# Kernel tuning notes

Measured on AMD Instinct MI355X. Metric: run time of the kernel, lower is better.

Reference implementation:

```python
import jax, jax.numpy as jnp
import numpy as np


def setup_inputs() -> dict:
    key = jax.random.key(0)
    B, S, H, D = 4, 2048, 16, 64
    kq, kk, kv, kl = jax.random.split(key, 4)
    q = jax.random.normal(kq, (B, S, H, D), dtype=jnp.float32)
    k = jax.random.normal(kk, (B, S, H, D), dtype=jnp.float32)
    v = jax.random.normal(kv, (B, S, H, D), dtype=jnp.float32)
    # varlen: each sequence has a valid prefix length in [S//2, S]
    lengths = jax.random.randint(kl, (B,), S // 2, S + 1)
    key_padding_mask = jnp.arange(S)[None, :] < lengths[:, None]  # [B, S] bool
    return {"q": q, "k": k, "v": v, "key_padding_mask": key_padding_mask}


def reference(q, k, v, key_padding_mask):
    # q,k,v: [B, S, H, D]; key_padding_mask: [B, S] (True = valid key/value token).
    # Equivalent math of ring varlen flash attention: every query attends to all
    # valid (unpadded) key positions of its sequence; padded keys are excluded.
    D = q.shape[-1]
    scale = 1.0 / np.sqrt(D).astype(np.float32)
    scores = jnp.einsum('bshd,bthd->bhst', q, k) * scale  # [B, H, S, S]
    neg = jnp.finfo(scores.dtype).min
    scores = jnp.where(key_padding_mask[:, None, None, :], scores, neg)
    probs = jax.nn.softmax(scores, axis=-1)
    context = jnp.einsum('bhst,bthd->bshd', probs, v)  # [B, S, H, D]
    return context
```

## Files before the change

kernel.cpp:

```cpp
#include <hip/hip_runtime.h>

#define BB 4
#define SS 2048
#define HH 16
#define DD 64

#define NQW 8
#define QW  32
#define QB  (NQW*QW)
#define KVB 32

#define KRS 144
#define VRS 80

typedef short bf16x8 __attribute__((ext_vector_type(8)));
typedef float f32x16 __attribute__((ext_vector_type(16)));

__device__ __forceinline__ unsigned cvtpk(float lo, float hi){
    unsigned r;
    asm("v_cvt_pk_bf16_f32 %0, %1, %2" : "=v"(r) : "v"(lo), "v"(hi));
    return r;
}

#if __has_builtin(__builtin_amdgcn_exp2f)
#define EXP2F(x) __builtin_amdgcn_exp2f(x)
#else
__device__ __forceinline__ float exp2_asm(float x){
    float r; asm("v_exp_f32 %0, %1\n\ts_nop 0" : "=v"(r) : "v"(x)); return r;
}
#define EXP2F(x) exp2_asm(x)
#endif

union FragU { unsigned u[4]; bf16x8 v; };

__global__ __launch_bounds__(512)
void attn_mfma(const float* __restrict__ qg, const float* __restrict__ kg,
               const float* __restrict__ vg, const int* __restrict__ maskg,
               float* __restrict__ outg)
{
    __shared__ __align__(16) unsigned char kl_raw[2][KVB*KRS];
    __shared__ __align__(16) unsigned char vt_raw[2][DD*VRS];
    __shared__ int lsum_s[NQW];

    const int i0 = (int)blockIdx.x;
    const int x  = i0 & 7;
    const int j  = i0 >> 3;
    const int qt = (j >> 2) & 7;
    const int b  = (x + j + (j >> 5)) & 3;
    const int h  = ((j >> 5) << 3) | x;

    const int t    = (int)threadIdx.x;
    const int wid  = t >> 6;
    const int lane = t & 63;
    const int lq   = lane & 31;
    const int lh   = lane >> 5;

    const int* mrow = maskg + b*SS;
    int part = 0;
    #pragma unroll
    for (int i = 0; i < 4; ++i) part += mrow[t*4 + i];
    #pragma unroll
    for (int off = 1; off < 64; off <<= 1) part += __shfl_xor(part, off);
    if (lane == 0) lsum_s[wid] = part;
    __syncthreads();
    int L = 0;
    #pragma unroll
    for (int w = 0; w < NQW; ++w) L += lsum_s[w];
    const int nt = (L + KVB - 1) / KVB;

    const int q0 = qt*QB + wid*QW + lq;
    const float* qrow = qg + ((size_t)((size_t)b*SS + q0)*HH + h)*DD;
    const float QSC = 0.125f * 1.44269504088896340736f;
    bf16x8 Qh[4];
    #pragma unroll
    for (int kc = 0; kc < 4; ++kc) {
        const float* p = qrow + kc*16 + lh*8;
        float4 a = *(const float4*)p;
        float4 c4 = *(const float4*)(p + 4);
        FragU f;
        f.u[0] = cvtpk(a.x*QSC, a.y*QSC);
        f.u[1] = cvtpk(a.z*QSC, a.w*QSC);
        f.u[2] = cvtpk(c4.x*QSC, c4.y*QSC);
        f.u[3] = cvtpk(c4.z*QSC, c4.w*QSC);
        Qh[kc] = f.v;
    }

    f32x16 O0, O1, ZERO;
    #pragma unroll
    for (int i = 0; i < 16; ++i) { O0[i]=0.f; O1[i]=0.f; ZERO[i]=0.f; }
    float lp = 0.f;

    const size_t kvstride = (size_t)HH*DD;
    const float* kbase = kg + ((size_t)b*SS*HH + h)*(size_t)DD;
    const float* vbase = vg + ((size_t)b*SS*HH + h)*(size_t)DD;

    const int skr  = t >> 4;
    const int sc4  = (t & 15) * 4;
    const int blkp = ((skr >> 2) ^ (skr >> 3)) & 1;
    const int pskr = skr ^ (blkp ? 12 : 0);
    const int skp  = t & 15;
    const int d0v  = (t >> 4) * 2;

    float kx[4], va_[2], vb_[2];

    auto LOADT = [&](int kt0) {
        const float* kp = kbase + (size_t)(kt0 + skr)*kvstride + sc4;
        float4 a = *(const float4*)kp;
        kx[0]=a.x; kx[1]=a.y; kx[2]=a.z; kx[3]=a.w;
        const float* vp0 = vbase + (size_t)(kt0 + 2*skp)*kvstride + d0v;
        const float* vp1 = vp0 + kvstride;
        float2 d2 = *(const float2*)vp0;
        float2 e2 = *(const float2*)vp1;
        va_[0]=d2.x; va_[1]=d2.y;
        vb_[0]=e2.x; vb_[1]=e2.y;
    };

    auto CVTW = [&](int bsel) {
        uint2 kf;
        kf.x = cvtpk(kx[0], kx[1]);
        kf.y = cvtpk(kx[2], kx[3]);
        unsigned koff = (unsigned)pskr*KRS + (unsigned)sc4*2u;
        koff ^= ((unsigned)(pskr>>3)&3u) << 4;
        *(uint2*)(kl_raw[bsel] + koff) = kf;
        #pragma unroll
        for (int i2 = 0; i2 < 2; ++i2) {
            unsigned dw = cvtpk(va_[i2], vb_[i2]);
            *(unsigned*)(vt_raw[bsel] + (unsigned)(d0v + i2)*VRS + (unsigned)skp*4u) = dw;
        }
    };

    LOADT(0);
    CVTW(0);

    for (int it = 0; it < nt; ++it) {
        __syncthreads();
        const int  cur  = it & 1;
        const bool more = (it + 1 < nt);

        const unsigned char* vtb = vt_raw[cur];
        FragU v00, v10, v01, v11;
        v00.v = *(const bf16x8*)(vtb + (unsigned)lq*VRS + (unsigned)(lh*16));
        v10.v = *(const bf16x8*)(vtb + (unsigned)(lq+32)*VRS + (unsigned)(lh*16));
        v01.v = *(const bf16x8*)(vtb + (unsigned)lq*VRS + (unsigned)(32 + lh*16));
        v11.v = *(const bf16x8*)(vtb + (unsigned)(lq+32)*VRS + (unsigned)(32 + lh*16));

        if (more) LOADT((it + 1) * KVB);

        const unsigned char* klb = kl_raw[cur];
        __builtin_amdgcn_s_setprio(1);
        FragU kf0;
        {
            unsigned off = (unsigned)lq*KRS + (unsigned)(lh*16);
            off ^= ((unsigned)(lq>>3)&3u) << 4;
            kf0.v = *(const bf16x8*)(klb + off);
        }
        f32x16 S = __builtin_amdgcn_mfma_f32_32x32x16_bf16(kf0.v, Qh[0], ZERO, 0, 0, 0);
        #pragma unroll
        for (int kc = 1; kc < 4; ++kc) {
            unsigned off = (unsigned)lq*KRS + (unsigned)(kc*32 + lh*16);
            off ^= ((unsigned)(lq>>3)&3u) << 4;
            FragU kf;
            kf.v = *(const bf16x8*)(klb + off);
            S = __builtin_amdgcn_mfma_f32_32x32x16_bf16(kf.v, Qh[kc], S, 0, 0, 0);
        }
        __builtin_amdgcn_s_setprio(0);

        const int kt0 = it * KVB;
        if (kt0 + KVB > L) {
            #pragma unroll
            for (int r = 0; r < 16; ++r) {
                const int key = kt0 + r + 8*(r>>3) + 8*lh;
                if (key >= L) S[r] = -1e30f;
            }
        }

        float p[16];
        #pragma unroll
        for (int r = 0; r < 16; ++r) p[r] = EXP2F(S[r]);

        float s0 = (p[0] + p[1]) + (p[2] + p[3]);
        float s1 = (p[4] + p[5]) + (p[6] + p[7]);
        float s2 = (p[8] + p[9]) + (p[10] + p[11]);
        float s3 = (p[12] + p[13]) + (p[14] + p[15]);
        lp += (s0 + s1) + (s2 + s3);

        FragU B0, B1;
        B0.u[0] = cvtpk(p[0],  p[1]);  B0.u[1] = cvtpk(p[2],  p[3]);
        B0.u[2] = cvtpk(p[4],  p[5]);  B0.u[3] = cvtpk(p[6],  p[7]);
        B1.u[0] = cvtpk(p[8],  p[9]);  B1.u[1] = cvtpk(p[10], p[11]);
        B1.u[2] = cvtpk(p[12], p[13]); B1.u[3] = cvtpk(p[14], p[15]);

        __builtin_amdgcn_s_setprio(1);
        O0 = __builtin_amdgcn_mfma_f32_32x32x16_bf16(v00.v, B0.v, O0, 0, 0, 0);
        O1 = __builtin_amdgcn_mfma_f32_32x32x16_bf16(v10.v, B0.v, O1, 0, 0, 0);
        O0 = __builtin_amdgcn_mfma_f32_32x32x16_bf16(v01.v, B1.v, O0, 0, 0, 0);
        O1 = __builtin_amdgcn_mfma_f32_32x32x16_bf16(v11.v, B1.v, O1, 0, 0, 0);
        __builtin_amdgcn_s_setprio(0);

        if (more) CVTW(cur ^ 1);
    }

    lp += __shfl_xor(lp, 32);
    const float inv = 1.0f / lp;
    float* orow = outg + ((size_t)((size_t)b*SS + q0)*HH + h)*DD;
    #pragma unroll
    for (int run = 0; run < 4; ++run) {
        float4 w0, w1;
        w0.x = O0[4*run+0]*inv; w0.y = O0[4*run+1]*inv;
        w0.z = O0[4*run+2]*inv; w0.w = O0[4*run+3]*inv;
        w1.x = O1[4*run+0]*inv; w1.y = O1[4*run+1]*inv;
        w1.z = O1[4*run+2]*inv; w1.w = O1[4*run+3]*inv;
        *(float4*)(orow + 8*run + 4*lh)      = w0;
        *(float4*)(orow + 32 + 8*run + 4*lh) = w1;
    }
}

extern "C" void kernel_launch(void* const* d_in, const int* in_sizes, int n_in,
                              void* d_out, int out_size, void* d_ws, size_t ws_size,
                              hipStream_t stream) {
    const float* q    = (const float*)d_in[0];
    const float* k    = (const float*)d_in[1];
    const float* v    = (const float*)d_in[2];
    const int*   mask = (const int*)d_in[3];
    float* out = (float*)d_out;

    dim3 grid(BB * HH * (SS / QB));
    dim3 block(512);
    hipLaunchKernelGGL(attn_mfma, grid, block, 0, stream, q, k, v, mask, out);
}
```

Baseline: 77.48 us.

## Double KV tile to 64 keys per iteration with two interleaved score MFMA chains

Raises the KV tile from 32 to 64 keys per loop iteration. Each iteration now computes two independent 32-key score accumulators, which interleaves their MFMA chains, and the global K/V loads widen to 8- and 4-float vectors. The aim is to halve the number of barriers and loop iterations and to expose more instruction-level parallelism. In exchange it uses more LDS and registers, and tail masking now applies to a coarser 64-key granularity, so more padded keys get computed and discarded.

```diff
diff --git a/kernel.cpp b/kernel.cpp
--- a/kernel.cpp
+++ b/kernel.cpp
@@ -8,10 +8,11 @@
 #define NQW 8
 #define QW  32
 #define QB  (NQW*QW)
-#define KVB 32
+#define KVB 64
 
 #define KRS 144
-#define VRS 80
+#define KSUB (32*KRS)
+#define VRS 144
 
 typedef short bf16x8 __attribute__((ext_vector_type(8)));
 typedef float f32x16 __attribute__((ext_vector_type(16)));
@@ -38,7 +39,7 @@
                const float* __restrict__ vg, const int* __restrict__ maskg,
                float* __restrict__ outg)
 {
-    __shared__ __align__(16) unsigned char kl_raw[2][KVB*KRS];
+    __shared__ __align__(16) unsigned char kl_raw[2][2*KSUB];
     __shared__ __align__(16) unsigned char vt_raw[2][DD*VRS];
     __shared__ int lsum_s[NQW];
 
@@ -66,7 +67,7 @@
     int L = 0;
     #pragma unroll
     for (int w = 0; w < NQW; ++w) L += lsum_s[w];
-    const int nt = (L + KVB - 1) / KVB;
+    const int nt64 = (L + KVB - 1) / KVB;
 
     const int q0 = qt*QB + wid*QW + lq;
     const float* qrow = qg + ((size_t)((size_t)b*SS + q0)*HH + h)*DD;
@@ -85,45 +86,48 @@
         Qh[kc] = f.v;
     }
 
-    f32x16 O0, O1, ZERO;
-    #pragma unroll
-    for (int i = 0; i < 16; ++i) { O0[i]=0.f; O1[i]=0.f; ZERO[i]=0.f; }
+    f32x16 O0, O1;
+    #pragma unroll
+    for (int i = 0; i < 16; ++i) { O0[i]=0.f; O1[i]=0.f; }
     float lp = 0.f;
 
     const size_t kvstride = (size_t)HH*DD;
     const float* kbase = kg + ((size_t)b*SS*HH + h)*(size_t)DD;
     const float* vbase = vg + ((size_t)b*SS*HH + h)*(size_t)DD;
 
-    const int skr  = t >> 4;
-    const int sc4  = (t & 15) * 4;
-    const int blkp = ((skr >> 2) ^ (skr >> 3)) & 1;
-    const int pskr = skr ^ (blkp ? 12 : 0);
-    const int skp  = t & 15;
-    const int d0v  = (t >> 4) * 2;
-
-    float kx[4], va_[2], vb_[2];
+    const int skr  = t >> 3;
+    const int sc8  = (t & 7) * 8;
+    const int ksub = skr >> 5;
+    const int r32  = skr & 31;
+    const int blkp = ((r32 >> 2) ^ (r32 >> 3)) & 1;
+    const int pskr = r32 ^ (blkp ? 12 : 0);
+    const int skp  = t & 31;
+    const int d0v  = (t >> 5) * 4;
+
+    float kx[8], va_[4], vb_[4];
 
     auto LOADT = [&](int kt0) {
-        const float* kp = kbase + (size_t)(kt0 + skr)*kvstride + sc4;
-        float4 a = *(const float4*)kp;
+        const float* kp = kbase + (size_t)(kt0 + skr)*kvstride + sc8;
+        float4 a = *(const float4*)kp;  float4 c4 = *(const float4*)(kp + 4);
         kx[0]=a.x; kx[1]=a.y; kx[2]=a.z; kx[3]=a.w;
+        kx[4]=c4.x; kx[5]=c4.y; kx[6]=c4.z; kx[7]=c4.w;
         const float* vp0 = vbase + (size_t)(kt0 + 2*skp)*kvstride + d0v;
         const float* vp1 = vp0 + kvstride;
-        float2 d2 = *(const float2*)vp0;
-        float2 e2 = *(const float2*)vp1;
-        va_[0]=d2.x; va_[1]=d2.y;
-        vb_[0]=e2.x; vb_[1]=e2.y;
+        float4 d4 = *(const float4*)vp0;
+        float4 e4 = *(const float4*)vp1;
+        va_[0]=d4.x; va_[1]=d4.y; va_[2]=d4.z; va_[3]=d4.w;
+        vb_[0]=e4.x; vb_[1]=e4.y; vb_[2]=e4.z; vb_[3]=e4.w;
     };
 
     auto CVTW = [&](int bsel) {
-        uint2 kf;
-        kf.x = cvtpk(kx[0], kx[1]);
-        kf.y = cvtpk(kx[2], kx[3]);
-        unsigned koff = (unsigned)pskr*KRS + (unsigned)sc4*2u;
+        FragU kf;
+        #pragma unroll
+        for (int jj = 0; jj < 4; ++jj) kf.u[jj] = cvtpk(kx[2*jj], kx[2*jj+1]);
+        unsigned koff = (unsigned)ksub*KSUB + (unsigned)pskr*KRS + (unsigned)sc8*2u;
         koff ^= ((unsigned)(pskr>>3)&3u) << 4;
-        *(uint2*)(kl_raw[bsel] + koff) = kf;
-        #pragma unroll
-        for (int i2 = 0; i2 < 2; ++i2) {
+        *(bf16x8*)(kl_raw[bsel] + koff) = kf.v;
+        #pragma unroll
+        for (int i2 = 0; i2 < 4; ++i2) {
             unsigned dw = cvtpk(va_[i2], vb_[i2]);
             *(unsigned*)(vt_raw[bsel] + (unsigned)(d0v + i2)*VRS + (unsigned)skp*4u) = dw;
         }
@@ -132,70 +136,101 @@
     LOADT(0);
     CVTW(0);
 
-    for (int it = 0; it < nt; ++it) {
+    for (int it = 0; it < nt64; ++it) {
         __syncthreads();
         const int  cur  = it & 1;
-        const bool more = (it + 1 < nt);
-
+        const bool more = (it + 1 < nt64);
+        const int  kt0  = it * KVB;
+
+        const unsigned char* klb = kl_raw[cur];
         const unsigned char* vtb = vt_raw[cur];
-        FragU v00, v10, v01, v11;
-        v00.v = *(const bf16x8*)(vtb + (unsigned)lq*VRS + (unsigned)(lh*16));
-        v10.v = *(const bf16x8*)(vtb + (unsigned)(lq+32)*VRS + (unsigned)(lh*16));
-        v01.v = *(const bf16x8*)(vtb + (unsigned)lq*VRS + (unsigned)(32 + lh*16));
-        v11.v = *(const bf16x8*)(vtb + (unsigned)(lq+32)*VRS + (unsigned)(32 + lh*16));
-
-        if (more) LOADT((it + 1) * KVB);
-
-        const unsigned char* klb = kl_raw[cur];
+
+        FragU vA00, vA10, vA01, vA11;
+        vA00.v = *(const bf16x8*)(vtb + (unsigned)lq*VRS + (unsigned)(lh*16));
+        vA10.v = *(const bf16x8*)(vtb + (unsigned)(lq+32)*VRS + (unsigned)(lh*16));
+        vA01.v = *(const bf16x8*)(vtb + (unsigned)lq*VRS + (unsigned)(32 + lh*16));
+        vA11.v = *(const bf16x8*)(vtb + (unsigned)(lq+32)*VRS + (unsigned)(32 + lh*16));
+
+        if (more) LOADT(kt0 + KVB);
+
+        f32x16 SA, SB;
+        #pragma unroll
+        for (int i = 0; i < 16; ++i) { SA[i] = 0.f; SB[i] = 0.f; }
         __builtin_amdgcn_s_setprio(1);
-        FragU kf0;
-        {
-            unsigned off = (unsigned)lq*KRS + (unsigned)(lh*16);
-            off ^= ((unsigned)(lq>>3)&3u) << 4;
-            kf0.v = *(const bf16x8*)(klb + off);
-        }
-        f32x16 S = __builtin_amdgcn_mfma_f32_32x32x16_bf16(kf0.v, Qh[0], ZERO, 0, 0, 0);
-        #pragma unroll
-        for (int kc = 1; kc < 4; ++kc) {
-            unsigned off = (unsigned)lq*KRS + (unsigned)(kc*32 + lh*16);
-            off ^= ((unsigned)(lq>>3)&3u) << 4;
-            FragU kf;
-            kf.v = *(const bf16x8*)(klb + off);
-            S = __builtin_amdgcn_mfma_f32_32x32x16_bf16(kf.v, Qh[kc], S, 0, 0, 0);
+        #pragma unroll
+        for (int kc = 0; kc < 4; ++kc) {
+            unsigned offA = (unsigned)lq*KRS + (unsigned)(kc*32 + lh*16);
+            offA ^= ((unsigned)(lq>>3)&3u) << 4;
+            FragU kfa, kfb;
+            kfa.v = *(const bf16x8*)(klb + offA);
+            kfb.v = *(const bf16x8*)(klb + KSUB + offA);
+            SA = __builtin_amdgcn_mfma_f32_32x32x16_bf16(kfa.v, Qh[kc], SA, 0, 0, 0);
+            SB = __builtin_amdgcn_mfma_f32_32x32x16_bf16(kfb.v, Qh[kc], SB, 0, 0, 0);
         }
         __builtin_amdgcn_s_setprio(0);
 
-        const int kt0 = it * KVB;
         if (kt0 + KVB > L) {
             #pragma unroll
             for (int r = 0; r < 16; ++r) {
-                const int key = kt0 + r + 8*(r>>3) + 8*lh;
-                if (key >= L) S[r] = -1e30f;
+                const int base = kt0 + r + 8*(r>>3) + 8*lh;
+                if (base      >= L) SA[r] = -1e30f;
+                if (base + 32 >= L) SB[r] = -1e30f;
             }
         }
 
-        float p[16];
-        #pragma unroll
-        for (int r = 0; r < 16; ++r) p[r] = EXP2F(S[r]);
-
-        float s0 = (p[0] + p[1]) + (p[2] + p[3]);
-        float s1 = (p[4] + p[5]) + (p[6] + p[7]);
-        float s2 = (p[8] + p[9]) + (p[10] + p[11]);
-        float s3 = (p[12] + p[13]) + (p[14] + p[15]);
-        lp += (s0 + s1) + (s2 + s3);
-
-        FragU B0, B1;
-        B0.u[0] = cvtpk(p[0],  p[1]);  B0.u[1] = cvtpk(p[2],  p[3]);
-        B0.u[2] = cvtpk(p[4],  p[5]);  B0.u[3] = cvtpk(p[6],  p[7]);
-        B1.u[0] = cvtpk(p[8],  p[9]);  B1.u[1] = cvtpk(p[10], p[11]);
-        B1.u[2] = cvtpk(p[12], p[13]); B1.u[3] = cvtpk(p[14], p[15]);
-
-        __builtin_amdgcn_s_setprio(1);
-        O0 = __builtin_amdgcn_mfma_f32_32x32x16_bf16(v00.v, B0.v, O0, 0, 0, 0);
-        O1 = __builtin_amdgcn_mfma_f32_32x32x16_bf16(v10.v, B0.v, O1, 0, 0, 0);
-        O0 = __builtin_amdgcn_mfma_f32_32x32x16_bf16(v01.v, B1.v, O0, 0, 0, 0);
-        O1 = __builtin_amdgcn_mfma_f32_32x32x16_bf16(v11.v, B1.v, O1, 0, 0, 0);
-        __builtin_amdgcn_s_setprio(0);
+        {
+            float p[16];
+            #pragma unroll
+            for (int r = 0; r < 16; ++r) p[r] = EXP2F(SA[r]);
+            float s0 = (p[0] + p[1]) + (p[2] + p[3]);
+            float s1 = (p[4] + p[5]) + (p[6] + p[7]);
+            float s2 = (p[8] + p[9]) + (p[10] + p[11]);
+            float s3 = (p[12] + p[13]) + (p[14] + p[15]);
+            lp += (s0 + s1) + (s2 + s3);
+
+            FragU B0, B1;
+            B0.u[0] = cvtpk(p[0],  p[1]);  B0.u[1] = cvtpk(p[2],  p[3]);
+            B0.u[2] = cvtpk(p[4],  p[5]);  B0.u[3] = cvtpk(p[6],  p[7]);
+            B1.u[0] = cvtpk(p[8],  p[9]);  B1.u[1] = cvtpk(p[10], p[11]);
+            B1.u[2] = cvtpk(p[12], p[13]); B1.u[3] = cvtpk(p[14], p[15]);
+
+            __builtin_amdgcn_s_setprio(1);
+            O0 = __builtin_amdgcn_mfma_f32_32x32x16_bf16(vA00.v, B0.v, O0, 0, 0, 0);
+            O1 = __builtin_amdgcn_mfma_f32_32x32x16_bf16(vA10.v, B0.v, O1, 0, 0, 0);
+            O0 = __builtin_amdgcn_mfma_f32_32x32x16_bf16(vA01.v, B1.v, O0, 0, 0, 0);
+            O1 = __builtin_amdgcn_mfma_f32_32x32x16_bf16(vA11.v, B1.v, O1, 0, 0, 0);
+            __builtin_amdgcn_s_setprio(0);
+        }
+
+        {
+            FragU vB00, vB10, vB01, vB11;
+            vB00.v = *(const bf16x8*)(vtb + (unsigned)lq*VRS + (unsigned)(64 + lh*16));
+            vB10.v = *(const bf16x8*)(vtb + (unsigned)(lq+32)*VRS + (unsigned)(64 + lh*16));
+            vB01.v = *(const bf16x8*)(vtb + (unsigned)lq*VRS + (unsigned)(96 + lh*16));
+            vB11.v = *(const bf16x8*)(vtb + (unsigned)(lq+32)*VRS + (unsigned)(96 + lh*16));
+
+            float p[16];
+            #pragma unroll
+            for (int r = 0; r < 16; ++r) p[r] = EXP2F(SB[r]);
+            float s0 = (p[0] + p[1]) + (p[2] + p[3]);
+            float s1 = (p[4] + p[5]) + (p[6] + p[7]);
+            float s2 = (p[8] + p[9]) + (p[10] + p[11]);
+            float s3 = (p[12] + p[13]) + (p[14] + p[15]);
+            lp += (s0 + s1) + (s2 + s3);
+
+            FragU B0, B1;
+            B0.u[0] = cvtpk(p[0],  p[1]);  B0.u[1] = cvtpk(p[2],  p[3]);
+            B0.u[2] = cvtpk(p[4],  p[5]);  B0.u[3] = cvtpk(p[6],  p[7]);
+            B1.u[0] = cvtpk(p[8],  p[9]);  B1.u[1] = cvtpk(p[10], p[11]);
+            B1.u[2] = cvtpk(p[12], p[13]); B1.u[3] = cvtpk(p[14], p[15]);
+
+            __builtin_amdgcn_s_setprio(1);
+            O0 = __builtin_amdgcn_mfma_f32_32x32x16_bf16(vB00.v, B0.v, O0, 0, 0, 0);
+            O1 = __builtin_amdgcn_mfma_f32_32x32x16_bf16(vB10.v, B0.v, O1, 0, 0, 0);
+            O0 = __builtin_amdgcn_mfma_f32_32x32x16_bf16(vB01.v, B1.v, O0, 0, 0, 0);
+            O1 = __builtin_amdgcn_mfma_f32_32x32x16_bf16(vB11.v, B1.v, O1, 0, 0, 0);
+            __builtin_amdgcn_s_setprio(0);
+        }
 
         if (more) CVTW(cur ^ 1);
     }
```

After: 86.50 us. 11.6% more time.
